# Kernel optimization log

Measured on AMD Instinct MI355X. Metric: run time of the kernel, lower is better.

The kernel has to match this reference:

```python
import jax, jax.numpy as jnp
import numpy as np

N_NODES = 100000


def gcn_conv(x, W, b, src, dst, n):
    """PyG GCNConv: symmetric-normalized aggregation with self-loops, then bias.
    x: [N, Fin], W: [Fin, Fout], b: [Fout], src/dst: [E].
    """
    h = x @ W  # [N, Fout]
    # degree with self-loops (edge weight 1.0), computed at destination (col)
    deg = jnp.zeros((n,), dtype=x.dtype).at[dst].add(1.0) + 1.0  # [N]
    dis = jax.lax.rsqrt(deg)  # deg^-1/2
    norm = dis[src] * dis[dst]  # [E]
    msg = h[src] * norm[:, None]  # [E, Fout] gather + scale
    agg = jax.ops.segment_sum(msg, dst, num_segments=n)  # scatter-add
    # self-loop contribution: norm_ii = deg_i^-1/2 * deg_i^-1/2 = 1/deg_i
    agg = agg + h * (1.0 / deg)[:, None]
    return agg + b


def setup_inputs() -> dict:
    key = jax.random.key(0)
    ks = jax.random.split(key, 10)
    n_dim = 256
    E = 400000
    x = jax.random.normal(ks[0], (N_NODES, n_dim), dtype=jnp.float32)
    edge_index = jax.random.randint(ks[1], (2, E), 0, N_NODES, dtype=jnp.int64)
    s = 0.05
    W1 = jax.random.normal(ks[2], (n_dim, 1024), dtype=jnp.float32) * s
    b1 = jnp.zeros((1024,), dtype=jnp.float32)
    W2 = jax.random.normal(ks[3], (1024, 512), dtype=jnp.float32) * s
    b2 = jnp.zeros((512,), dtype=jnp.float32)
    W3 = jax.random.normal(ks[4], (512, 128), dtype=jnp.float32) * s
    b3 = jnp.zeros((128,), dtype=jnp.float32)
    Wc = jax.random.normal(ks[5], (128, 100), dtype=jnp.float32) * s
    bc = jnp.zeros((100,), dtype=jnp.float32)
    return {"x": x, "edge_index": edge_index, "W1": W1, "b1": b1,
            "W2": W2, "b2": b2, "W3": W3, "b3": b3, "Wc": Wc, "bc": bc}


def reference(x, edge_index, W1, b1, W2, b2, W3, b3, Wc, bc):
    n = x.shape[0]
    src, dst = edge_index[0], edge_index[1]
    h = jnp.tanh(gcn_conv(x, W1, b1, src, dst, n))
    h = jnp.tanh(gcn_conv(h, W2, b2, src, dst, n))
    h = jnp.tanh(gcn_conv(h, W3, b3, src, dst, n))
    out = jax.nn.sigmoid(h @ Wc + bc)
    return (out, h)
```

## Files before the change

kernel.cpp:

```cpp
#include <hip/hip_runtime.h>
#include <stdint.h>

typedef long long ll;
typedef unsigned short u16;
typedef __attribute__((ext_vector_type(8))) short bf16x8;
typedef __attribute__((ext_vector_type(4))) float f32x4;

__device__ inline bool ei_is64(const void* ei) {
  const int* p = (const int*)ei;
  return ((p[1] | p[3] | p[5] | p[7]) == 0);
}
__device__ inline int ei_at(const void* ei, ll i, bool is64) {
  return is64 ? (int)((const ll*)ei)[i] : ((const int*)ei)[i];
}

__device__ inline float fast_tanh(float x) {
  x = fminf(15.f, fmaxf(-15.f, x));
  float e2 = __expf(2.f * x);
  return (e2 - 1.f) / (e2 + 1.f);
}
__device__ inline float fast_sigmoid(float x) { return 1.f / (1.f + __expf(-x)); }

__device__ inline float bf2f(u16 u) {
  union { unsigned int i; float f; } v; v.i = ((unsigned int)u) << 16; return v.f;
}
__device__ inline u16 f2bf(float f) {
  union { float f; unsigned int i; } v; v.f = f;
  unsigned int r = v.i + 0x7FFFu + ((v.i >> 16) & 1u);
  return (u16)(r >> 16);
}

__device__ inline void gload16(const u16* g, void* l) {
  __builtin_amdgcn_global_load_lds(
      (const __attribute__((address_space(1))) unsigned int*)(const void*)g,
      (__attribute__((address_space(3))) unsigned int*)l, 16, 0, 0);
}

__global__ void k_init(float* deg, int* cursor, int n) {
  int i = blockIdx.x * blockDim.x + threadIdx.x;
  if (i < n) { deg[i] = 1.0f; cursor[i] = 0; }
}
__global__ void k_edge_deg(const void* __restrict__ ei, ll E, float* deg) {
  ll i = (ll)blockIdx.x * blockDim.x + threadIdx.x;
  if (i >= E) return;
  bool is64 = ei_is64(ei);
  atomicAdd(&deg[ei_at(ei, E + i, is64)], 1.0f);
}
__global__ void k_fin_deg(const float* __restrict__ deg, float* __restrict__ isd,
                          float* __restrict__ invd, int n) {
  int i = blockIdx.x * blockDim.x + threadIdx.x;
  if (i < n) {
    float d = deg[i];
    isd[i] = rsqrtf(d);
    invd[i] = 1.0f / d;
  }
}

__global__ __launch_bounds__(1024) void k_scan1(const float* __restrict__ deg,
                                                int* __restrict__ rowp,
                                                int* __restrict__ part, int n) {
  __shared__ int sm[1024];
  int b = blockIdx.x, tid = threadIdx.x;
  int i = b * 1024 + tid;
  int v = (i < n) ? ((int)deg[i] - 1) : 0;
  sm[tid] = v;
  __syncthreads();
  for (int off = 1; off < 1024; off <<= 1) {
    int t = (tid >= off) ? sm[tid - off] : 0;
    __syncthreads();
    sm[tid] += t;
    __syncthreads();
  }
  if (i < n) rowp[i + 1] = sm[tid];
  if (tid == 1023) part[b] = sm[1023];
}
__global__ void k_scan2(const int* __restrict__ part, int* __restrict__ offs, int nb) {
  __shared__ int sm[128];
  int t = threadIdx.x;
  int v = (t < nb) ? part[t] : 0;
  sm[t] = v;
  __syncthreads();
  for (int off = 1; off < 128; off <<= 1) {
    int u = (t >= off) ? sm[t - off] : 0;
    __syncthreads();
    sm[t] += u;
    __syncthreads();
  }
  offs[t] = sm[t] - v;
}
__global__ __launch_bounds__(1024) void k_scan3(int* __restrict__ rowp,
                                                const int* __restrict__ offs, int n) {
  int i = blockIdx.x * 1024 + threadIdx.x;
  if (i == 0) rowp[0] = 0;
  if (i < n) rowp[i + 1] += offs[blockIdx.x];
}

__global__ void k_fill(const void* __restrict__ ei, ll E,
                       const int* __restrict__ rowp, int* __restrict__ cursor,
                       int* __restrict__ col, float* __restrict__ w,
                       const float* __restrict__ isd) {
  ll i = (ll)blockIdx.x * blockDim.x + threadIdx.x;
  if (i >= E) return;
  bool is64 = ei_is64(ei);
  int s = ei_at(ei, i, is64);
  int d = ei_at(ei, E + i, is64);
  int pos = rowp[d] + atomicAdd(&cursor[d], 1);
  col[pos] = s;
  w[pos] = isd[s] * isd[d];
}

__global__ void k_wt(const float* __restrict__ W, u16* __restrict__ Wt, int K, int N) {
  int t = blockIdx.x * blockDim.x + threadIdx.x;
  if (t >= K * N) return;
  int k = t % K, n = t / K;
  Wt[t] = f2bf(W[(size_t)k * N + n]);
}
__global__ void k_wtc(const float* __restrict__ W, u16* __restrict__ Wt, int K, int N) {
  int t = blockIdx.x * blockDim.x + threadIdx.x;
  if (t >= 128 * K) return;
  int k = t % K, n = t / K;
  Wt[t] = (n < N) ? f2bf(W[(size_t)k * N + n]) : (u16)0;
}

template <int EPI, int OBF, int OB2>
__global__ void k_gather(const int* __restrict__ rowp, const int* __restrict__ col,
                         const float* __restrict__ w,
                         const float* __restrict__ in, int ldin,
                         const float* __restrict__ invd, const float* __restrict__ bias,
                         void* __restrict__ outv, u16* __restrict__ out2,
                         int n, int lgC) {
  ll gid = (ll)blockIdx.x * blockDim.x + threadIdx.x;
  ll total = (ll)n << lgC;
  if (gid >= total) return;
  int d = (int)(gid >> lgC);
  int c4 = (int)(gid & ((1 << lgC) - 1));
  float4 acc;
  {
    float4 v = *(const float4*)(in + (size_t)d * ldin + c4 * 4);
    float s = invd[d];
    acc.x = v.x * s; acc.y = v.y * s; acc.z = v.z * s; acc.w = v.w * s;
  }
  int b = rowp[d], e = rowp[d + 1];
  for (int j = b; j < e; ++j) {
    int s = col[j];
    float wt = w[j];
    float4 v = *(const float4*)(in + (size_t)s * ldin + c4 * 4);
    acc.x += wt * v.x; acc.y += wt * v.y; acc.z += wt * v.z; acc.w += wt * v.w;
  }
  if (EPI == 1) {
    int c = c4 * 4;
    acc.x = fast_tanh(acc.x + bias[c + 0]);
    acc.y = fast_tanh(acc.y + bias[c + 1]);
    acc.z = fast_tanh(acc.z + bias[c + 2]);
    acc.w = fast_tanh(acc.w + bias[c + 3]);
  }
  if (OBF) {
    ushort4 o;
    o.x = f2bf(acc.x); o.y = f2bf(acc.y); o.z = f2bf(acc.z); o.w = f2bf(acc.w);
    ((ushort4*)outv)[gid] = o;
  } else {
    ((float4*)outv)[gid] = acc;
  }
  if (OB2) {
    ushort4 o;
    o.x = f2bf(acc.x); o.y = f2bf(acc.y); o.z = f2bf(acc.z); o.w = f2bf(acc.w);
    ((ushort4*)out2)[gid] = o;
  }
}

template <int CPB, int CACC, int EPI, int OBF, bool CG>
__global__ __launch_bounds__(256) void k_mfma2(const u16* __restrict__ A, int ldA,
                                               const u16* __restrict__ Bt, int ldB,
                                               const float* __restrict__ bias,
                                               void* __restrict__ Cv, int ldC,
                                               int M, int K, int SPX, int GZ, int NC) {
  int bid = blockIdx.x;
  int xcd = bid & 7, j = bid >> 3;
  int by = xcd * SPX + j / CPB;
  int bx = j % CPB;
  if (by >= GZ) return;

  __shared__ char As[2 * 16384];

  const int tid = threadIdx.x;
  const int lane = tid & 63;
  const int w = tid >> 6;
  const int wm = w >> 1, wn = w & 1;
  const int rb = by * 128;
  const int c0 = bx * 128 + wn * 64;
  const int lr = lane & 15;
  const int kg = lane >> 4;

  f32x4 acc[4][4];
#pragma unroll
  for (int i = 0; i < 4; ++i)
#pragma unroll
    for (int jj = 0; jj < 4; ++jj) acc[i][jj] = (f32x4)0.f;

  const u16* bp[4];
#pragma unroll
  for (int fn = 0; fn < 4; ++fn)
    bp[fn] = Bt + (size_t)(c0 + fn * 16 + lr) * ldB + kg * 8;

  int aoff[2][4];
#pragma unroll
  for (int ks = 0; ks < 2; ++ks)
#pragma unroll
    for (int fm = 0; fm < 4; ++fm) {
      int row = wm * 64 + fm * 16 + lr;
      int slot = (ks * 4 + kg) ^ (row & 7);
      aoff[ks][fm] = row * 128 + slot * 16;
    }

  auto STAGE = [&](int buf, int k0) {
#pragma unroll
    for (int it = 0; it < 4; ++it) {
      int li = it * 256 + tid;
      int row = li >> 3;
      int slot = li & 7;
      int gr = rb + row;
      if (gr > M - 1) gr = M - 1;
      int gk = k0 + ((slot ^ (row & 7)) << 3);
      char* dst = As + buf * 16384 + it * 4096 + w * 1024;
      gload16(A + (size_t)gr * ldA + gk, dst);
    }
  };

  const int nt = K >> 6;
  STAGE(0, 0);
  __syncthreads();
  int cur = 0;
  for (int t = 0; t < nt; ++t) {
    if (t + 1 < nt) STAGE(cur ^ 1, (t + 1) << 6);
    const char* ab = As + cur * 16384;
    const int k0 = t << 6;
#pragma unroll
    for (int ks = 0; ks < 2; ++ks) {
      bf16x8 a[4], b[4];
#pragma unroll
      for (int i = 0; i < 4; ++i) a[i] = *(const bf16x8*)(ab + aoff[ks][i]);
#pragma unroll
      for (int i = 0; i < 4; ++i) b[i] = *(const bf16x8*)(bp[i] + k0 + ks * 32);
#pragma unroll
      for (int fm = 0; fm < 4; ++fm)
#pragma unroll
        for (int fn = 0; fn < 4; ++fn)
          acc[fm][fn] = __builtin_amdgcn_mfma_f32_16x16x32_bf16(a[fm], b[fn], acc[fm][fn], 0, 0, 0);
    }
    __syncthreads();
    cur ^= 1;
  }

  const int orow = kg * 4;
  const int ocol = lane & 15;
#pragma unroll
  for (int fm = 0; fm < 4; ++fm) {
#pragma unroll
    for (int jj = 0; jj < 4; ++jj) {
      int gr = rb + wm * 64 + fm * 16 + orow + jj;
      if (gr >= M) continue;
#pragma unroll
      for (int fn = 0; fn < 4; ++fn) {
        int gc = c0 + fn * 16 + ocol;
        if (CG && gc >= NC) continue;
        float v = acc[fm][fn][jj];
        size_t off = (size_t)gr * ldC + gc;
        if (CACC) v += ((const float*)Cv)[off];
        if (EPI == 1) v = fast_tanh(v + bias[gc]);
        if (EPI == 2) v = fast_sigmoid(v + bias[gc]);
        if (OBF) ((u16*)Cv)[off] = f2bf(v);
        else     ((float*)Cv)[off] = v;
      }
    }
  }
}

static inline int cdiv(ll a, ll b) { return (int)((a + b - 1) / b); }

extern "C" void kernel_launch(void* const* d_in, const int* in_sizes, int n_in,
                              void* d_out, int out_size, void* d_ws, size_t ws_size,
                              hipStream_t stream) {
  const float* x  = (const float*)d_in[0];
  const void*  ei = d_in[1];
  const float* W1 = (const float*)d_in[2];
  const float* b1 = (const float*)d_in[3];
  const float* W2 = (const float*)d_in[4];
  const float* b2 = (const float*)d_in[5];
  const float* W3 = (const float*)d_in[6];
  const float* b3 = (const float*)d_in[7];
  const float* Wc = (const float*)d_in[8];
  const float* bc = (const float*)d_in[9];

  const int Nn = in_sizes[0] / 256;
  const ll  E  = in_sizes[1] / 2;

  u16*   h1  = (u16*)d_ws;
  float* q3  = (float*)((char*)d_ws + (size_t)Nn * 2048);
  u16*   hb  = (u16*)d_ws;
  u16*   Wct = (u16*)((char*)d_ws + 32u * 1024 * 1024);

  float* ob     = (float*)d_out;
  float* deg    = ob;
  float* isd    = ob + Nn;
  float* invd   = ob + 2 * (size_t)Nn;
  int*   rowp   = (int*)(ob + 3 * (size_t)Nn);
  int*   cursor = (int*)(ob + 4 * (size_t)Nn + 4);
  int*   colx   = (int*)(ob + 5 * (size_t)Nn + 8);
  float* wgt    = ob + 5 * (size_t)Nn + 8 + E;
  int*   part   = (int*)(ob + 5 * (size_t)Nn + 8 + 2 * E);
  int*   offs   = part + 128;
  u16*   W1t    = (u16*)(offs + 128);
  u16*   W2t    = W1t + 1024 * 256;
  u16*   W3t    = W2t + 512 * 1024;
  float* stA    = ob + 1800000;
  u16*   stB    = (u16*)(ob + 14600000);
  float* outf   = ob;
  float* hout   = ob + (size_t)Nn * 100;

  const int T = 256;
  const int GZ = cdiv(Nn, 128);
  const int SPX = cdiv(GZ, 8);
  const int SB = cdiv(Nn, 1024);

  k_init<<<cdiv(Nn, T), T, 0, stream>>>(deg, cursor, Nn);
  k_edge_deg<<<cdiv(E, T), T, 0, stream>>>(ei, E, deg);
  k_fin_deg<<<cdiv(Nn, T), T, 0, stream>>>(deg, isd, invd, Nn);
  k_scan1<<<SB, 1024, 0, stream>>>(deg, rowp, part, Nn);
  k_scan2<<<1, 128, 0, stream>>>(part, offs, SB);
  k_scan3<<<SB, 1024, 0, stream>>>(rowp, offs, Nn);
  k_fill<<<cdiv(E, T), T, 0, stream>>>(ei, E, rowp, cursor, colx, wgt, isd);
  k_wt<<<cdiv(256 * 1024, T), T, 0, stream>>>(W1, W1t, 256, 1024);
  k_wt<<<cdiv(1024 * 512, T), T, 0, stream>>>(W2, W2t, 1024, 512);
  k_wt<<<cdiv(512 * 128, T), T, 0, stream>>>(W3, W3t, 512, 128);

  {
    ll t4 = (ll)Nn * 64;
    k_gather<0, 1, 0><<<cdiv(t4, T), T, 0, stream>>>(rowp, colx, wgt, x, 256, invd,
                                                     nullptr, stA, nullptr, Nn, 6);
    k_mfma2<8, 0, 1, 1, false><<<8 * SPX * 8, T, 0, stream>>>(
        (const u16*)stA, 256, W1t, 256, b1, h1, 1024, Nn, 256, SPX, GZ, 1024);
  }

  for (int c = 0; c < 4; ++c) {
    const int c0 = c * 128;
    k_mfma2<1, 0, 0, 0, false><<<8 * SPX, T, 0, stream>>>(
        h1, 1024, W2t + (size_t)c0 * 1024, 1024, nullptr, stA, 128, Nn, 1024, SPX, GZ, 128);
    ll t4 = (ll)Nn * 32;
    k_gather<1, 1, 0><<<cdiv(t4, T), T, 0, stream>>>(rowp, colx, wgt, stA, 128, invd,
                                                     b2 + c0, stB, nullptr, Nn, 5);
    if (c == 0)
      k_mfma2<1, 0, 0, 0, false><<<8 * SPX, T, 0, stream>>>(
          stB, 128, W3t + c0, 512, nullptr, q3, 128, Nn, 128, SPX, GZ, 128);
    else
      k_mfma2<1, 1, 0, 0, false><<<8 * SPX, T, 0, stream>>>(
          stB, 128, W3t + c0, 512, nullptr, q3, 128, Nn, 128, SPX, GZ, 128);
  }

  {
    ll t4 = (ll)Nn * 32;
    k_gather<1, 0, 1><<<cdiv(t4, T), T, 0, stream>>>(rowp, colx, wgt, q3, 128, invd,
                                                     b3, hout, hb, Nn, 5);
  }

  {
    k_wtc<<<cdiv(128 * 128, T), T, 0, stream>>>(Wc, Wct, 128, 100);
    k_mfma2<1, 0, 2, 0, true><<<8 * SPX, T, 0, stream>>>(
        hb, 128, Wct, 128, bc, outf, 100, Nn, 128, SPX, GZ, 100);
  }
}
```

Measured before the change: 1.285 ms.

## Stage B tiles in LDS, store layer-2 projection as bf16, widen column chunks

```diff
diff --git a/kernel.cpp b/kernel.cpp
--- a/kernel.cpp
+++ b/kernel.cpp
@@ -122,10 +122,10 @@
   Wt[t] = (n < N) ? f2bf(W[(size_t)k * N + n]) : (u16)0;
 }
 
-template <int EPI, int OBF, int OB2>
+template <int EPI, int OBF, int OB2, int IBF>
 __global__ void k_gather(const int* __restrict__ rowp, const int* __restrict__ col,
                          const float* __restrict__ w,
-                         const float* __restrict__ in, int ldin,
+                         const void* __restrict__ inv, int ldin,
                          const float* __restrict__ invd, const float* __restrict__ bias,
                          void* __restrict__ outv, u16* __restrict__ out2,
                          int n, int lgC) {
@@ -134,9 +134,21 @@
   if (gid >= total) return;
   int d = (int)(gid >> lgC);
   int c4 = (int)(gid & ((1 << lgC) - 1));
+
+  auto load4 = [&](int r) -> float4 {
+    if (IBF) {
+      ushort4 uv = *(const ushort4*)((const u16*)inv + (size_t)r * ldin + c4 * 4);
+      float4 f;
+      f.x = bf2f(uv.x); f.y = bf2f(uv.y); f.z = bf2f(uv.z); f.w = bf2f(uv.w);
+      return f;
+    } else {
+      return *(const float4*)((const float*)inv + (size_t)r * ldin + c4 * 4);
+    }
+  };
+
   float4 acc;
   {
-    float4 v = *(const float4*)(in + (size_t)d * ldin + c4 * 4);
+    float4 v = load4(d);
     float s = invd[d];
     acc.x = v.x * s; acc.y = v.y * s; acc.z = v.z * s; acc.w = v.w * s;
   }
@@ -144,7 +156,7 @@
   for (int j = b; j < e; ++j) {
     int s = col[j];
     float wt = w[j];
-    float4 v = *(const float4*)(in + (size_t)s * ldin + c4 * 4);
+    float4 v = load4(s);
     acc.x += wt * v.x; acc.y += wt * v.y; acc.z += wt * v.z; acc.w += wt * v.w;
   }
   if (EPI == 1) {
@@ -175,19 +187,21 @@
                                                void* __restrict__ Cv, int ldC,
                                                int M, int K, int SPX, int GZ, int NC) {
   int bid = blockIdx.x;
-  int xcd = bid & 7, j = bid >> 3;
-  int by = xcd * SPX + j / CPB;
-  int bx = j % CPB;
+  int xcd = bid & 7, j0 = bid >> 3;
+  int by = xcd * SPX + j0 / CPB;
+  int bx = j0 % CPB;
   if (by >= GZ) return;
 
-  __shared__ char As[2 * 16384];
+  __shared__ char LdsA[32768];
+  __shared__ char LdsB[32768];
 
   const int tid = threadIdx.x;
   const int lane = tid & 63;
   const int w = tid >> 6;
   const int wm = w >> 1, wn = w & 1;
   const int rb = by * 128;
-  const int c0 = bx * 128 + wn * 64;
+  const int cb = bx * 128;
+  const int c0 = cb + wn * 64;
   const int lr = lane & 15;
   const int kg = lane >> 4;
 
@@ -197,58 +211,56 @@
 #pragma unroll
     for (int jj = 0; jj < 4; ++jj) acc[i][jj] = (f32x4)0.f;
 
-  const u16* bp[4];
-#pragma unroll
-  for (int fn = 0; fn < 4; ++fn)
-    bp[fn] = Bt + (size_t)(c0 + fn * 16 + lr) * ldB + kg * 8;
-
-  int aoff[2][4];
+  int alane[2];
 #pragma unroll
   for (int ks = 0; ks < 2; ++ks)
-#pragma unroll
-    for (int fm = 0; fm < 4; ++fm) {
-      int row = wm * 64 + fm * 16 + lr;
-      int slot = (ks * 4 + kg) ^ (row & 7);
-      aoff[ks][fm] = row * 128 + slot * 16;
-    }
+    alane[ks] = lr * 128 + (((ks * 4 + kg) ^ (lr & 7)) * 16);
+
+  const int srow = tid >> 3;
+  const int sk = ((tid & 7) ^ (srow & 7)) * 8;
+  const u16* aSrc[4];
+#pragma unroll
+  for (int it = 0; it < 4; ++it) {
+    int gr = rb + it * 32 + srow;
+    if (gr > M - 1) gr = M - 1;
+    aSrc[it] = A + (size_t)gr * ldA + sk;
+  }
+  const u16* bSrc = Bt + (size_t)(cb + srow) * ldB + sk;
+  const size_t bStep = (size_t)32 * ldB;
 
   auto STAGE = [&](int buf, int k0) {
 #pragma unroll
     for (int it = 0; it < 4; ++it) {
-      int li = it * 256 + tid;
-      int row = li >> 3;
-      int slot = li & 7;
-      int gr = rb + row;
-      if (gr > M - 1) gr = M - 1;
-      int gk = k0 + ((slot ^ (row & 7)) << 3);
-      char* dst = As + buf * 16384 + it * 4096 + w * 1024;
-      gload16(A + (size_t)gr * ldA + gk, dst);
+      gload16(aSrc[it] + k0, LdsA + buf * 16384 + it * 4096 + w * 1024);
+      gload16(bSrc + (size_t)it * bStep + k0, LdsB + buf * 16384 + it * 4096 + w * 1024);
+    }
+  };
+
+  auto COMPUTE = [&](int buf) {
+    const char* ab = LdsA + buf * 16384 + ((wm * 64) << 7);
+    const char* bb = LdsB + buf * 16384 + ((wn * 64) << 7);
+#pragma unroll
+    for (int ks = 0; ks < 2; ++ks) {
+      bf16x8 a[4], b[4];
+#pragma unroll
+      for (int i = 0; i < 4; ++i) a[i] = *(const bf16x8*)(ab + (i << 11) + alane[ks]);
+#pragma unroll
+      for (int i = 0; i < 4; ++i) b[i] = *(const bf16x8*)(bb + (i << 11) + alane[ks]);
+#pragma unroll
+      for (int fm = 0; fm < 4; ++fm)
+#pragma unroll
+        for (int fn = 0; fn < 4; ++fn)
+          acc[fm][fn] = __builtin_amdgcn_mfma_f32_16x16x32_bf16(a[fm], b[fn], acc[fm][fn], 0, 0, 0);
     }
   };
 
   const int nt = K >> 6;
   STAGE(0, 0);
   __syncthreads();
-  int cur = 0;
   for (int t = 0; t < nt; ++t) {
-    if (t + 1 < nt) STAGE(cur ^ 1, (t + 1) << 6);
-    const char* ab = As + cur * 16384;
-    const int k0 = t << 6;
-#pragma unroll
-    for (int ks = 0; ks < 2; ++ks) {
-      bf16x8 a[4], b[4];
-#pragma unroll
-      for (int i = 0; i < 4; ++i) a[i] = *(const bf16x8*)(ab + aoff[ks][i]);
-#pragma unroll
-      for (int i = 0; i < 4; ++i) b[i] = *(const bf16x8*)(bp[i] + k0 + ks * 32);
-#pragma unroll
-      for (int fm = 0; fm < 4; ++fm)
-#pragma unroll
-        for (int fn = 0; fn < 4; ++fn)
-          acc[fm][fn] = __builtin_amdgcn_mfma_f32_16x16x32_bf16(a[fm], b[fn], acc[fm][fn], 0, 0, 0);
-    }
-    __syncthreads();
-    cur ^= 1;
+    if (t + 1 < nt) STAGE((t + 1) & 1, (t + 1) << 6);
+    COMPUTE(t & 1);
+    __syncthreads();
   }
 
   const int orow = kg * 4;
@@ -312,8 +324,8 @@
   u16*   W1t    = (u16*)(offs + 128);
   u16*   W2t    = W1t + 1024 * 256;
   u16*   W3t    = W2t + 512 * 1024;
-  float* stA    = ob + 1800000;
-  u16*   stB    = (u16*)(ob + 14600000);
+  u16*   qc     = (u16*)(ob + 1800000);
+  u16*   h2s    = (u16*)(ob + 14600000);
   float* outf   = ob;
   float* hout   = ob + (size_t)Nn * 100;
 
@@ -335,31 +347,34 @@
 
   {
     ll t4 = (ll)Nn * 64;
-    k_gather<0, 1, 0><<<cdiv(t4, T), T, 0, stream>>>(rowp, colx, wgt, x, 256, invd,
-                                                     nullptr, stA, nullptr, Nn, 6);
+    k_gather<0, 1, 0, 0><<<cdiv(t4, T), T, 0, stream>>>(rowp, colx, wgt, x, 256, invd,
+                                                        nullptr, qc, nullptr, Nn, 6);
     k_mfma2<8, 0, 1, 1, false><<<8 * SPX * 8, T, 0, stream>>>(
-        (const u16*)stA, 256, W1t, 256, b1, h1, 1024, Nn, 256, SPX, GZ, 1024);
-  }
-
-  for (int c = 0; c < 4; ++c) {
-    const int c0 = c * 128;
-    k_mfma2<1, 0, 0, 0, false><<<8 * SPX, T, 0, stream>>>(
-        h1, 1024, W2t + (size_t)c0 * 1024, 1024, nullptr, stA, 128, Nn, 1024, SPX, GZ, 128);
-    ll t4 = (ll)Nn * 32;
-    k_gather<1, 1, 0><<<cdiv(t4, T), T, 0, stream>>>(rowp, colx, wgt, stA, 128, invd,
-                                                     b2 + c0, stB, nullptr, Nn, 5);
-    if (c == 0)
-      k_mfma2<1, 0, 0, 0, false><<<8 * SPX, T, 0, stream>>>(
-          stB, 128, W3t + c0, 512, nullptr, q3, 128, Nn, 128, SPX, GZ, 128);
-    else
-      k_mfma2<1, 1, 0, 0, false><<<8 * SPX, T, 0, stream>>>(
-          stB, 128, W3t + c0, 512, nullptr, q3, 128, Nn, 128, SPX, GZ, 128);
+        qc, 256, W1t, 256, b1, h1, 1024, Nn, 256, SPX, GZ, 1024);
+  }
+
+  for (int c = 0; c < 2; ++c) {
+    k_mfma2<2, 0, 0, 1, false><<<8 * SPX * 2, T, 0, stream>>>(
+        h1, 1024, W2t + (size_t)(c * 256) * 1024, 1024, nullptr, qc, 256, Nn, 1024,
+        SPX, GZ, 256);
+    for (int s = 0; s < 2; ++s) {
+      const int k0 = c * 256 + s * 128;
+      ll t4 = (ll)Nn * 32;
+      k_gather<1, 1, 0, 1><<<cdiv(t4, T), T, 0, stream>>>(
+          rowp, colx, wgt, qc + s * 128, 256, invd, b2 + k0, h2s, nullptr, Nn, 5);
+      if (k0 == 0)
+        k_mfma2<1, 0, 0, 0, false><<<8 * SPX, T, 0, stream>>>(
+            h2s, 128, W3t + k0, 512, nullptr, q3, 128, Nn, 128, SPX, GZ, 128);
+      else
+        k_mfma2<1, 1, 0, 0, false><<<8 * SPX, T, 0, stream>>>(
+            h2s, 128, W3t + k0, 512, nullptr, q3, 128, Nn, 128, SPX, GZ, 128);
+    }
   }
 
   {
     ll t4 = (ll)Nn * 32;
-    k_gather<1, 0, 1><<<cdiv(t4, T), T, 0, stream>>>(rowp, colx, wgt, q3, 128, invd,
-                                                     b3, hout, hb, Nn, 5);
+    k_gather<1, 0, 1, 0><<<cdiv(t4, T), T, 0, stream>>>(rowp, colx, wgt, q3, 128, invd,
+                                                        b3, hout, hb, Nn, 5);
   }
 
   {
```

New measurement: 1.051 ms. 18.2% less time.
